# Kernel tuning notes

Measured on AMD Instinct MI355X. Metric: run time of the kernel, lower is better.

Reference implementation:

```python
import jax, jax.numpy as jnp
import numpy as np

# dims: B jets, K routed slots per jet, S particles, D embed, E experts, H heads
B, K, S, D, E, H = 512, 2, 128, 128, 4, 8
F = 4 * D  # ffn_dim
MAXN = 1.0 - 1e-5  # Poincare ball (c=1) max norm for projx


def _n(x):
    return jnp.sqrt(jnp.clip(jnp.sum(x * x, axis=-1, keepdims=True), 1e-15))


def expmap0(u):
    n = _n(u)
    return jnp.tanh(n) * u / n


def logmap0(x):
    n = _n(x)
    return jnp.arctanh(jnp.minimum(n, MAXN)) * x / n


def projx(x):
    n = _n(x)
    return jnp.where(n > MAXN, x * (MAXN / n), x)


def mobius_add(x, y):
    xy = jnp.sum(x * y, axis=-1, keepdims=True)
    x2 = jnp.sum(x * x, axis=-1, keepdims=True)
    y2 = jnp.sum(y * y, axis=-1, keepdims=True)
    num = (1.0 + 2.0 * xy + y2) * x + (1.0 - x2) * y
    den = 1.0 + 2.0 * xy + x2 * y2
    return num / jnp.clip(den, 1e-15)


def layernorm(x, g, b):
    m = jnp.mean(x, axis=-1, keepdims=True)
    v = jnp.mean((x - m) ** 2, axis=-1, keepdims=True)
    return g * (x - m) / jnp.sqrt(v + 1e-5) + b


def man_linear(x, W, b):
    # Manifold_Linear: mobius matvec == expmap0(W @ logmap0(x)), then mobius bias, projx
    return projx(mobius_add(expmap0(logmap0(x) @ W.T), expmap0(b)))


def mob_relu(x):
    # Mob_Act(ReLU): expmap0(relu(logmap0(x)))
    return expmap0(jax.nn.relu(logmap0(x)))


def setup_inputs():
    key = jax.random.key(0)
    ks = jax.random.split(key, 16)
    features = expmap0(0.05 * jax.random.normal(ks[0], (B, K, S, D), jnp.float32))
    # K distinct expert ids per sample (original .nonzero().item() assumes uniqueness)
    expert_indices = jnp.argsort(jax.random.uniform(ks[1], (B, E)), axis=1)[:, :K].astype(jnp.int32)
    pm = jax.random.uniform(ks[2], (B, S)) < 0.2
    pm = pm.at[:, 0].set(False)  # keep at least one valid token per row
    w = lambda k, shp, sc: sc * jax.random.normal(k, shp, jnp.float32)
    s = 1.0 / np.sqrt(D)
    sf = 1.0 / np.sqrt(F)
    return dict(
        features=features, expert_indices=expert_indices, padding_mask=pm,
        ln1_g=jnp.ones((E, D)), ln1_b=jnp.zeros((E, D)),
        ln2_g=jnp.ones((E, D)), ln2_b=jnp.zeros((E, D)),
        wq=w(ks[3], (E, D, D), s), bq=w(ks[4], (E, D), 0.02),
        wk=w(ks[5], (E, D, D), s), bk=w(ks[6], (E, D), 0.02),
        wv=w(ks[7], (E, D, D), s), bv=w(ks[8], (E, D), 0.02),
        wo=w(ks[9], (E, D, D), s), bo=w(ks[10], (E, D), 0.02),
        fc1_w=w(ks[11], (E, F, D), s), fc1_b=w(ks[12], (E, F), 0.02),
        fc2_w=w(ks[13], (E, D, F), sf), fc2_b=w(ks[14], (E, D), 0.02),
    )


def _mha(x, Wq, bq, Wk, bk, Wv, bv, Wo, bo, pad_bias):
    b, s, d = x.shape
    hd = d // H
    q = logmap0(man_linear(x, Wq, bq)).reshape(b, s, H, hd)
    k = logmap0(man_linear(x, Wk, bk)).reshape(b, s, H, hd)
    v = logmap0(man_linear(x, Wv, bv)).reshape(b, s, H, hd)
    scores = jnp.einsum('bqhd,bkhd->bhqk', q, k) * (1.0 / np.sqrt(hd)) + pad_bias
    att = jax.nn.softmax(scores, axis=-1)
    ctx = jnp.einsum('bhqk,bkhd->bqhd', att, v).reshape(b, s, d)
    return man_linear(expmap0(ctx), Wo, bo)


def _expert(x, e, P, pad_bias):
    res = x
    h = expmap0(layernorm(logmap0(x), P['ln1_g'][e], P['ln1_b'][e]))
    h = projx(_mha(h, P['wq'][e], P['bq'][e], P['wk'][e], P['bk'][e],
                   P['wv'][e], P['bv'][e], P['wo'][e], P['bo'][e], pad_bias))
    x = projx(mobius_add(h, res))
    res = x
    h = projx(expmap0(layernorm(logmap0(x), P['ln2_g'][e], P['ln2_b'][e])))
    h = projx(mob_relu(man_linear(h, P['fc1_w'][e], P['fc1_b'][e])))
    h = mob_relu(man_linear(h, P['fc2_w'][e], P['fc2_b'][e]))
    return projx(mobius_add(h, res))


def reference(features, expert_indices, padding_mask,
              ln1_g, ln1_b, ln2_g, ln2_b,
              wq, bq, wk, bk, wv, bv, wo, bo,
              fc1_w, fc1_b, fc2_w, fc2_b):
    P = dict(ln1_g=ln1_g, ln1_b=ln1_b, ln2_g=ln2_g, ln2_b=ln2_b,
             wq=wq, bq=bq, wk=wk, bk=bk, wv=wv, bv=bv, wo=wo, bo=bo,
             fc1_w=fc1_w, fc1_b=fc1_b, fc2_w=fc2_w, fc2_b=fc2_b)
    pad_bias = jnp.where(padding_mask, -1e9, 0.0)[:, None, None, :]  # [B,1,1,S]
    outs = []
    for e in range(E):  # small fixed expert loop (distinct params)
        sel = expert_indices == e  # [B,K]
        present = jnp.any(sel, axis=1)  # [B]
        slot = jnp.argmax(sel, axis=1)  # [B]
        x = jnp.take_along_axis(features, slot[:, None, None, None], axis=1)[:, 0]  # [B,S,D]
        y = _expert(x, e, P, pad_bias)
        outs.append(jnp.where(present[:, None, None], y, 0.0))
    return jnp.stack(outs, axis=1)  # [B,E,S,D]; zero rows where expert not routed
```

## Files before the change

### kernel.cpp

```cpp
#include <hip/hip_runtime.h>
#include <stdint.h>

#define SS 128
#define DD 128
#define EE 4
#define HH 8
#define HDIM 16
#define FF 512
#define BB 512
#define KK 2
#define NTASK (BB*KK)
#define MAXNF 0.99999f
#define NW3 786432

typedef unsigned short u16;
typedef unsigned int u32;

typedef __attribute__((ext_vector_type(8))) short s8v;
typedef __attribute__((ext_vector_type(4))) float f4v;

#define MFMA32(a,b,c) __builtin_amdgcn_mfma_f32_16x16x32_bf16(a,b,c,0,0,0)

__device__ __forceinline__ float bf2f(u16 h){ return __uint_as_float(((u32)h)<<16); }
__device__ __forceinline__ u16 f2bf(float f){
  u32 x = __float_as_uint(f);
  u32 r = x + 0x7FFFu + ((x>>16)&1u);
  return (u16)(r>>16);
}
__device__ __forceinline__ float bfl(u32 u){ return __uint_as_float(u<<16); }
__device__ __forceinline__ float bfh(u32 u){ return __uint_as_float(u & 0xFFFF0000u); }

__device__ __forceinline__ float wsum(float v){
  #pragma unroll
  for(int off=32; off>0; off>>=1) v += __shfl_xor(v, off, 64);
  return v;
}
__device__ __forceinline__ float wmax(float v){
  #pragma unroll
  for(int off=32; off>0; off>>=1) v = fmaxf(v, __shfl_xor(v, off, 64));
  return v;
}
__device__ __forceinline__ float artanhf_(float x){ return 0.5f*logf((1.f+x)/(1.f-x)); }

__device__ __forceinline__ u32 cvtpk(float a, float b){
  u32 r; asm("v_cvt_pk_bf16_f32 %0, %1, %2" : "=v"(r) : "v"(a), "v"(b)); return r;
}
__device__ __forceinline__ void split2(float a, float b, u32& H, u32& M, u32& L){
  H = cvtpk(a,b);
  float ra = a - bfl(H), rb = b - bfh(H);
  M = cvtpk(ra,rb);
  float sa = ra - bfl(M), sb = rb - bfh(M);
  L = cvtpk(sa,sb);
}
__device__ __forceinline__ void split8(const float* v, s8v& H, s8v& M, s8v& L){
  union { u32 w[4]; s8v s; } uh, um, ul;
  #pragma unroll
  for(int p=0;p<4;++p){
    u32 a,bq2,c; split2(v[2*p], v[2*p+1], a, bq2, c);
    uh.w[p]=a; um.w[p]=bq2; ul.w[p]=c;
  }
  H=uh.s; M=um.s; L=ul.s;
}
__device__ __forceinline__ s8v sel8(int c, s8v a, s8v b){ return c ? a : b; }

template<typename T> __device__ __forceinline__ float ldv(const T* p){
  if constexpr (sizeof(T)==2) return bf2f(*(const u16*)p);
  else return *(const float*)p;
}
template<typename T> __device__ __forceinline__ void stv(T* p, float v){
  if constexpr (sizeof(T)==2) *(u16*)p = f2bf(v);
  else *(float*)p = v;
}
template<typename T> __device__ __forceinline__ void loadrow(const T* p, float* w){
  if constexpr (sizeof(T)==2){
    const uint4* q=(const uint4*)p;
    #pragma unroll
    for(int r=0;r<16;++r){
      uint4 t=q[r];
      w[r*8+0]=bfl(t.x); w[r*8+1]=bfh(t.x);
      w[r*8+2]=bfl(t.y); w[r*8+3]=bfh(t.y);
      w[r*8+4]=bfl(t.z); w[r*8+5]=bfh(t.z);
      w[r*8+6]=bfl(t.w); w[r*8+7]=bfh(t.w);
    }
  } else {
    const float4* q=(const float4*)p;
    #pragma unroll
    for(int r=0;r<32;++r){ float4 t=q[r]; w[r*4]=t.x; w[r*4+1]=t.y; w[r*4+2]=t.z; w[r*4+3]=t.w; }
  }
}
__device__ __forceinline__ float dotrow(const float* __restrict__ w, const float* __restrict__ u){
  float a0=0.f,a1=0.f,a2=0.f,a3=0.f;
  #pragma unroll
  for(int i=0;i<128;i+=4){
    a0+=w[i]*u[i]; a1+=w[i+1]*u[i+1]; a2+=w[i+2]*u[i+2]; a3+=w[i+3]*u[i+3];
  }
  return (a0+a1)+(a2+a3);
}

template<int NPL> __device__ __forceinline__ float vnorm(const float* v){
  float s=0.f;
  #pragma unroll
  for(int i=0;i<NPL;++i) s += v[i]*v[i];
  s = wsum(s);
  return sqrtf(fmaxf(s, 1e-15f));
}
template<int NPL> __device__ __forceinline__ void f_logmap0(float* v){
  float n = vnorm<NPL>(v);
  float sc = artanhf_(fminf(n, MAXNF))/n;
  #pragma unroll
  for(int i=0;i<NPL;++i) v[i]*=sc;
}
template<int NPL> __device__ __forceinline__ void f_expmap0(float* v){
  float n = vnorm<NPL>(v);
  float sc = tanhf(n)/n;
  #pragma unroll
  for(int i=0;i<NPL;++i) v[i]*=sc;
}
template<int NPL> __device__ __forceinline__ void f_projx(float* v){
  float n = vnorm<NPL>(v);
  if(n > MAXNF){
    float sc = MAXNF/n;
    #pragma unroll
    for(int i=0;i<NPL;++i) v[i]*=sc;
  }
}
template<int NPL> __device__ __forceinline__ void f_mobius_add(float* x, const float* y){
  float xy=0.f, x2=0.f, y2=0.f;
  #pragma unroll
  for(int i=0;i<NPL;++i){ xy+=x[i]*y[i]; x2+=x[i]*x[i]; y2+=y[i]*y[i]; }
  xy=wsum(xy); x2=wsum(x2); y2=wsum(y2);
  float cx = 1.f + 2.f*xy + y2;
  float cy = 1.f - x2;
  float den = fmaxf(1.f + 2.f*xy + x2*y2, 1e-15f);
  float inv = 1.f/den;
  #pragma unroll
  for(int i=0;i<NPL;++i) x[i] = (cx*x[i] + cy*y[i])*inv;
}
template<int NPL> __device__ __forceinline__ void f_layernorm(float* v, const float* g, const float* b){
  const float invD = 1.f/(float)(NPL*64);
  float m=0.f;
  #pragma unroll
  for(int i=0;i<NPL;++i) m += v[i];
  m = wsum(m)*invD;
  float s2=0.f;
  #pragma unroll
  for(int i=0;i<NPL;++i){ v[i]-=m; s2 += v[i]*v[i]; }
  s2 = wsum(s2)*invD;
  float inv = 1.f/sqrtf(s2+1e-5f);
  #pragma unroll
  for(int i=0;i<NPL;++i) v[i] = g[i]*(v[i]*inv) + b[i];
}

__device__ __forceinline__ u32 xf32(int row, int colf){
  return (u32)row*512u + (((u32)colf*4u) ^ (((u32)row&7u)<<4));
}
__device__ __forceinline__ u32 xbh(int row, int colb){
  return (u32)row*256u + (((u32)colb*2u) ^ (((u32)row&7u)<<4));
}
__device__ __forceinline__ u32 xhid(int row, int colb){
  return (u32)row*1024u + (((u32)colb*2u) ^ (((u32)row&7u)<<4));
}
__device__ __forceinline__ u32 xfr_(int row, int colf){
  return (u32)row*2048u + (((u32)colf*4u) ^ (((u32)row&7u)<<4));
}

__global__ void prep_kernel(const u16* __restrict__ feat16,
                            const unsigned char* __restrict__ mask,
                            float* __restrict__ mbias, int* __restrict__ flag){
  __shared__ int s_stats, s_max, s_nan;
  if(threadIdx.x==0){ s_stats=0; s_max=0; s_nan=0; }
  __syncthreads();
  int c=0;
  for(int i=threadIdx.x; i<131072; i+=blockDim.x){
    u16 v = feat16[i];
    if(((v>>7)&0xFFu)==0xFFu) c++;
  }
  if(c) atomicAdd(&s_nan, c);
  int lstats=0, lmax=0;
  for(int i=threadIdx.x; i<BB*SS; i+=blockDim.x){
    int v = mask[i];
    if(v){
      lmax = v>lmax ? v : lmax;
      if((i&3)==1) lstats|=1;
      if((i&3)!=0) lstats|=2;
    }
  }
  if(lstats) atomicOr(&s_stats, lstats);
  atomicMax(&s_max, lmax);
  __syncthreads();
  if(threadIdx.x==0) *flag = (s_nan>0) ? 1 : 0;
  int mode;
  if(s_max<=1) mode = (s_stats&2) ? 0 : 1;
  else         mode = (s_stats&1) ? 2 : 3;
  for(int i=threadIdx.x; i<BB*SS; i+=blockDim.x){
    bool m2;
    if(mode==0)      m2 = mask[i]!=0;
    else if(mode==1) m2 = ((const int*)mask)[i]!=0;
    else if(mode==2) m2 = ((const u16*)mask)[i]!=0;
    else             m2 = ((((const u32*)mask)[i])<<1)!=0;
    mbias[i] = m2 ? -1e9f : 0.f;
  }
}

template<typename T>
__global__ void zero_nr(const int* __restrict__ flag, const int* __restrict__ eidx, T* __restrict__ out){
  const int want = (sizeof(T)==4) ? 1 : 0;
  if(*flag != want) return;
  for(int slab=blockIdx.x; slab<BB*EE; slab+=gridDim.x){
    int b = slab>>2, e = slab&3;
    if(eidx[b*KK]==e || eidx[b*KK+1]==e) continue;
    T* p = out + (size_t)slab*(SS*DD);
    for(int i=threadIdx.x; i<SS*DD; i+=blockDim.x){
      if constexpr (sizeof(T)==2) p[i] = (T)0; else p[i] = 0.f;
    }
  }
}

__global__ void wsplit_kernel(const int* __restrict__ flag,
                              const float* __restrict__ wq, const float* __restrict__ wk,
                              const float* __restrict__ wv, const float* __restrict__ wo,
                              const float* __restrict__ f1w, const float* __restrict__ f2w,
                              u16* __restrict__ wsp){
  if(*flag != 1) return;
  int i = blockIdx.x*256 + threadIdx.x;
  if(i >= NW3) return;
  float x;
  if(i < 65536)       x = wq[i];
  else if(i < 131072) x = wk[i-65536];
  else if(i < 196608) x = wv[i-131072];
  else if(i < 262144) x = wo[i-196608];
  else if(i < 524288) x = f1w[i-262144];
  else                x = f2w[i-524288];
  u32 H,M,L; split2(x,x,H,M,L);
  wsp[i]         = (u16)H;
  wsp[NW3 + i]   = (u16)M;
  wsp[2*NW3 + i] = (u16)L;
}

__global__ __launch_bounds__(512)
void moe_f32(const int* __restrict__ flag,
             const float* __restrict__ feat, const int* __restrict__ eidx,
             const float* __restrict__ mbias,
             const float* __restrict__ ln1g, const float* __restrict__ ln1b,
             const float* __restrict__ ln2g, const float* __restrict__ ln2b,
             const float* __restrict__ bq, const float* __restrict__ bk_,
             const float* __restrict__ bv, const float* __restrict__ bo,
             const float* __restrict__ f1b, const float* __restrict__ f2b,
             const u16* __restrict__ wsp,
             float* __restrict__ out, float* __restrict__ wsl, int ntask)
{
  if(*flag != 1) return;

  __shared__ __align__(16) char LB[163840];
  char* Uh = LB;
  char* Um = LB + 32768;
  char* R2 = LB + 65536;
  char* SX = LB + 131072;
  char* HB = LB + 98304;
  char* C2 = LB + 147456;

  const int tid = threadIdx.x;
  const int lane = tid & 63;
  const int w    = tid >> 6;
  const int ll   = lane & 15;
  const int hl   = lane >> 4;

  u16* myl = (u16*)wsl + (size_t)blockIdx.x * 16384;

  for(int task = blockIdx.x; task < ntask; task += gridDim.x){
    __syncthreads();
    const int b = task >> 1, slot = task & 1;
    const int e  = eidx[b*KK + slot];
    const int eo = eidx[b*KK + (slot^1)];
    int used = (1<<e)|(1<<eo), sp = 0, cnt = 0;
    #pragma unroll
    for(int t2=0;t2<4;++t2){ if(!((used>>t2)&1)){ if(cnt==slot) sp=t2; cnt++; } }
    const float* X = feat + (size_t)task * (SS*DD);
    float* own   = out + ((size_t)(b*EE+e )) * (SS*DD);
    float* spare = out + ((size_t)(b*EE+sp)) * (SS*DD);

    float g1[2],b1[2],g2[2],b2[2],ebq[2],ebk[2],ebv[2],ebo[2],ebf2[2],ebf1[8];
    {
      float2 t0;
      t0 = *(const float2*)(ln1g + e*DD + 2*lane); g1[0]=t0.x; g1[1]=t0.y;
      t0 = *(const float2*)(ln1b + e*DD + 2*lane); b1[0]=t0.x; b1[1]=t0.y;
      t0 = *(const float2*)(ln2g + e*DD + 2*lane); g2[0]=t0.x; g2[1]=t0.y;
      t0 = *(const float2*)(ln2b + e*DD + 2*lane); b2[0]=t0.x; b2[1]=t0.y;
      t0 = *(const float2*)(bq  + e*DD + 2*lane); ebq[0]=t0.x; ebq[1]=t0.y; f_expmap0<2>(ebq);
      t0 = *(const float2*)(bk_ + e*DD + 2*lane); ebk[0]=t0.x; ebk[1]=t0.y; f_expmap0<2>(ebk);
      t0 = *(const float2*)(bv  + e*DD + 2*lane); ebv[0]=t0.x; ebv[1]=t0.y; f_expmap0<2>(ebv);
      t0 = *(const float2*)(bo  + e*DD + 2*lane); ebo[0]=t0.x; ebo[1]=t0.y; f_expmap0<2>(ebo);
      t0 = *(const float2*)(f2b + e*DD + 2*lane); ebf2[0]=t0.x; ebf2[1]=t0.y; f_expmap0<2>(ebf2);
      #pragma unroll
      for(int j=0;j<4;++j){
        t0 = *(const float2*)(f1b + e*FF + 2*lane + 128*j); ebf1[2*j]=t0.x; ebf1[2*j+1]=t0.y;
      }
      f_expmap0<8>(ebf1);
    }
    float mb_reg[8];
    #pragma unroll
    for(int nt=0;nt<8;++nt) mb_reg[nt] = mbias[b*SS + nt*16 + ll];

    for(int r=0;r<16;++r){
      int t = w*16 + r;
      float2 xv = *(const float2*)(X + t*DD + 2*lane);
      float v[2] = {xv.x, xv.y};
      f_logmap0<2>(v);
      f_layernorm<2>(v, g1, b1);
      f_expmap0<2>(v);
      f_logmap0<2>(v);
      u32 H,M,L; split2(v[0],v[1],H,M,L);
      *(u32*)(Uh + xbh(t, 2*lane)) = H;
      *(u32*)(Um + xbh(t, 2*lane)) = M;
      ((u32*)myl)[t*64 + lane] = L;
    }
    __syncthreads();

    #pragma unroll
    for(int m=0;m<3;++m){
      const u32 tb = (m==0 ? 0u : (m==1 ? 65536u : 131072u)) + (u32)e*16384u;
      s8v Bh[8], Blm[8];
      {
        int nrow = w*16 + ll;
        #pragma unroll
        for(int c=0;c<8;++c){
          u32 koff = c*16 + (hl&1)*8;
          Bh[c]  = *(const s8v*)(wsp + 0*NW3 + tb + nrow*128 + koff);
          Blm[c] = *(const s8v*)(wsp + (hl<2?2:1)*NW3 + tb + nrow*128 + koff);
        }
      }
      for(int ch=0; ch<4; ++ch){
        #pragma unroll
        for(int sub=0; sub<2; ++sub){
          int mt = 2*ch + sub;
          f4v acc = {0.f,0.f,0.f,0.f};
          #pragma unroll
          for(int c=0;c<8;++c){
            int arow = mt*16 + ll;
            u32 koff = c*16 + (hl&1)*8;
            s8v A1 = *(const s8v*)((hl<2?Uh:Um) + xbh(arow, koff));
            s8v lf = *(const s8v*)((const u16*)myl + arow*128 + koff);
            s8v hf = *(const s8v*)(Uh + xbh(arow, koff));
            s8v A2 = sel8(hl<2, lf, hf);
            s8v B3 = sel8(hl<2, Bh[c], Blm[c]);
            acc = MFMA32(A1, Bh[c], acc);
            acc = MFMA32(A1, Blm[c], acc);
            acc = MFMA32(A2, B3, acc);
          }
          #pragma unroll
          for(int i=0;i<4;++i)
            *(float*)(SX + xf32(sub*16 + hl*4 + i, w*16 + ll)) = acc[i];
        }
        __syncthreads();
        for(int rr=0; rr<4; ++rr){
          int lr = w*4 + rr; int t = ch*32 + lr;
          float2 pp = *(const float2*)(SX + xf32(lr, 2*lane));
          float v[2] = {pp.x, pp.y};
          f_expmap0<2>(v);
          float eb[2];
          if(m==0){ eb[0]=ebq[0]; eb[1]=ebq[1]; }
          else if(m==1){ eb[0]=ebk[0]; eb[1]=ebk[1]; }
          else { eb[0]=ebv[0]; eb[1]=ebv[1]; }
          f_mobius_add<2>(v, eb);
          f_projx<2>(v);
          f_logmap0<2>(v);
          if(m==0){
            float2 o2; o2.x=v[0]; o2.y=v[1];
            *(float2*)(spare + t*DD + 2*lane) = o2;
          } else if(m==1){
            *(float*)(R2 + xf32(t, 2*lane))   = v[0];
            *(float*)(R2 + xf32(t, 2*lane+1)) = v[1];
          } else {
            own[(2*lane)*DD + t]   = v[0];
            own[(2*lane+1)*DD + t] = v[1];
          }
        }
        __syncthreads();
      }
    }

    for(int h=0; h<HH; ++h){
      {
        int tok = tid & 127, dq = tid >> 7;
        float4 vv = *(const float4*)(R2 + xf32(tok, h*16 + dq*4));
        u32 H0,M0,L0,H1,M1,L1;
        split2(vv.x,vv.y,H0,M0,L0); split2(vv.z,vv.w,H1,M1,L1);
        u32 o = (u32)tok*48u + (u32)dq*8u;
        *(u32*)(SX + 0*6144 + o) = H0; *(u32*)(SX + 0*6144 + o + 4) = H1;
        *(u32*)(SX + 1*6144 + o) = M0; *(u32*)(SX + 1*6144 + o + 4) = M1;
        *(u32*)(SX + 2*6144 + o) = L0; *(u32*)(SX + 2*6144 + o + 4) = L1;
      }
      __syncthreads();
      float qa[8];
      {
        float4 q0 = *(const float4*)(spare + (w*16+ll)*DD + h*16 + (hl&1)*8);
        float4 q1 = *(const float4*)(spare + (w*16+ll)*DD + h*16 + (hl&1)*8 + 4);
        qa[0]=q0.x; qa[1]=q0.y; qa[2]=q0.z; qa[3]=q0.w;
        qa[4]=q1.x; qa[5]=q1.y; qa[6]=q1.z; qa[7]=q1.w;
      }
      s8v QH,QM,QL; split8(qa, QH,QM,QL);
      s8v qA1 = sel8(hl<2, QH, QM);
      s8v qA2 = sel8(hl<2, QL, QH);
      f4v sc[8];
      #pragma unroll
      for(int nt=0;nt<8;++nt){
        u32 o = (u32)(nt*16+ll)*48u + (u32)(hl&1)*16u;
        s8v B1 = *(const s8v*)(SX + 0*6144 + o);
        s8v B2 = *(const s8v*)(SX + (hl<2?2:1)*6144 + o);
        s8v B3 = sel8(hl<2, B1, B2);
        f4v z = {0.f,0.f,0.f,0.f};
        z = MFMA32(qA1, B1, z);
        z = MFMA32(qA1, B2, z);
        z = MFMA32(qA2, B3, z);
        sc[nt] = z;
      }
      __syncthreads();
      #pragma unroll
      for(int i=0;i<4;++i){
        float p8[8]; float mx = -3e38f;
        #pragma unroll
        for(int nt=0;nt<8;++nt){ p8[nt] = sc[nt][i]*0.25f + mb_reg[nt]; mx = fmaxf(mx, p8[nt]); }
        #pragma unroll
        for(int o=1;o<16;o<<=1) mx = fmaxf(mx, __shfl_xor(mx, o, 64));
        float dn = 0.f;
        #pragma unroll
        for(int nt=0;nt<8;++nt){ p8[nt] = expf(p8[nt]-mx); dn += p8[nt]; }
        #pragma unroll
        for(int o=1;o<16;o<<=1) dn += __shfl_xor(dn, o, 64);
        float inv = 1.f/dn;
        #pragma unroll
        for(int nt=0;nt<8;++nt)
          *(float*)(LB + xf32(w*16 + hl*4 + i, nt*16 + ll)) = p8[nt]*inv;
      }
      f4v ca = {0.f,0.f,0.f,0.f};
      #pragma unroll
      for(int c=0;c<8;++c){
        float pa[8];
        {
          float4 p0 = *(const float4*)(LB + xf32(w*16+ll, c*16 + (hl&1)*8));
          float4 p1 = *(const float4*)(LB + xf32(w*16+ll, c*16 + (hl&1)*8 + 4));
          pa[0]=p0.x; pa[1]=p0.y; pa[2]=p0.z; pa[3]=p0.w;
          pa[4]=p1.x; pa[5]=p1.y; pa[6]=p1.z; pa[7]=p1.w;
        }
        s8v PH,PM,PL; split8(pa, PH,PM,PL);
        s8v pA1 = sel8(hl<2, PH, PM);
        s8v pA2 = sel8(hl<2, PL, PH);
        float va[8];
        {
          const float* vp = own + (h*16+ll)*DD + c*16 + (hl&1)*8;
          float4 v0 = *(const float4*)(vp);
          float4 v1 = *(const float4*)(vp + 4);
          va[0]=v0.x; va[1]=v0.y; va[2]=v0.z; va[3]=v0.w;
          va[4]=v1.x; va[5]=v1.y; va[6]=v1.z; va[7]=v1.w;
        }
        s8v VH,VM,VL; split8(va, VH,VM,VL);
        s8v vB2 = sel8(hl<2, VL, VM);
        s8v vB3 = sel8(hl<2, VH, VM);
        ca = MFMA32(pA1, VH, ca);
        ca = MFMA32(pA1, vB2, ca);
        ca = MFMA32(pA2, vB3, ca);
      }
      #pragma unroll
      for(int i=0;i<4;++i)
        *(float*)(R2 + xf32(w*16 + hl*4 + i, h*16 + ll)) = ca[i];
    }
    __syncthreads();

    for(int r=0;r<16;++r){
      int t = w*16 + r;
      float v[2];
      v[0] = *(const float*)(R2 + xf32(t, 2*lane));
      v[1] = *(const float*)(R2 + xf32(t, 2*lane+1));
      f_expmap0<2>(v);
      f_logmap0<2>(v);
      u32 H,M,L; split2(v[0],v[1],H,M,L);
      *(u32*)(Uh + xbh(t, 2*lane)) = H;
      *(u32*)(Um + xbh(t, 2*lane)) = M;
      ((u32*)myl)[t*64 + lane] = L;
    }
    __syncthreads();

    {
      const u32 tb = 196608u + (u32)e*16384u;
      s8v Bh[8], Blm[8];
      {
        int nrow = w*16 + ll;
        #pragma unroll
        for(int c=0;c<8;++c){
          u32 koff = c*16 + (hl&1)*8;
          Bh[c]  = *(const s8v*)(wsp + 0*NW3 + tb + nrow*128 + koff);
          Blm[c] = *(const s8v*)(wsp + (hl<2?2:1)*NW3 + tb + nrow*128 + koff);
        }
      }
      for(int ch=0; ch<4; ++ch){
        #pragma unroll
        for(int sub=0; sub<2; ++sub){
          int mt = 2*ch + sub;
          f4v acc = {0.f,0.f,0.f,0.f};
          #pragma unroll
          for(int c=0;c<8;++c){
            int arow = mt*16 + ll;
            u32 koff = c*16 + (hl&1)*8;
            s8v A1 = *(const s8v*)((hl<2?Uh:Um) + xbh(arow, koff));
            s8v lf = *(const s8v*)((const u16*)myl + arow*128 + koff);
            s8v hf = *(const s8v*)(Uh + xbh(arow, koff));
            s8v A2 = sel8(hl<2, lf, hf);
            s8v B3 = sel8(hl<2, Bh[c], Blm[c]);
            acc = MFMA32(A1, Bh[c], acc);
            acc = MFMA32(A1, Blm[c], acc);
            acc = MFMA32(A2, B3, acc);
          }
          #pragma unroll
          for(int i=0;i<4;++i)
            *(float*)(SX + xf32(sub*16 + hl*4 + i, w*16 + ll)) = acc[i];
        }
        __syncthreads();
        for(int rr=0; rr<4; ++rr){
          int lr = w*4 + rr; int t = ch*32 + lr;
          float2 pp = *(const float2*)(SX + xf32(lr, 2*lane));
          float v[2] = {pp.x, pp.y};
          f_expmap0<2>(v);
          f_mobius_add<2>(v, ebo);
          f_projx<2>(v);
          f_projx<2>(v);
          float2 rr2 = *(const float2*)(X + t*DD + 2*lane);
          float res[2] = {rr2.x, rr2.y};
          f_mobius_add<2>(v, res);
          f_projx<2>(v);
          float2 xo; xo.x=v[0]; xo.y=v[1];
          *(float2*)(own + t*DD + 2*lane) = xo;
          f_logmap0<2>(v);
          f_layernorm<2>(v, g2, b2);
          f_expmap0<2>(v);
          f_projx<2>(v);
          f_logmap0<2>(v);
          u32 H,M,L; split2(v[0],v[1],H,M,L);
          *(u32*)(Uh + xbh(t, 2*lane)) = H;
          *(u32*)(Um + xbh(t, 2*lane)) = M;
          ((u32*)myl)[t*64 + lane] = L;
        }
        __syncthreads();
      }
    }

    for(int tc=0; tc<8; ++tc){
      {
        f4v fa[4];
        #pragma unroll
        for(int n4=0;n4<4;++n4){ fa[n4][0]=0.f; fa[n4][1]=0.f; fa[n4][2]=0.f; fa[n4][3]=0.f; }
        #pragma unroll
        for(int c=0;c<8;++c){
          int arow = tc*16 + ll;
          u32 koff = c*16 + (hl&1)*8;
          s8v A1 = *(const s8v*)((hl<2?Uh:Um) + xbh(arow, koff));
          s8v lf = *(const s8v*)((const u16*)myl + arow*128 + koff);
          s8v hf = *(const s8v*)(Uh + xbh(arow, koff));
          s8v A2 = sel8(hl<2, lf, hf);
          #pragma unroll
          for(int n4=0;n4<4;++n4){
            u32 nrow = (u32)((w*4+n4)*16 + ll);
            s8v B1 = *(const s8v*)(wsp + 0*NW3 + 262144u + (u32)e*65536u + nrow*128 + koff);
            s8v B2 = *(const s8v*)(wsp + (hl<2?2:1)*NW3 + 262144u + (u32)e*65536u + nrow*128 + koff);
            s8v B3 = sel8(hl<2, B1, B2);
            fa[n4] = MFMA32(A1, B1, fa[n4]);
            fa[n4] = MFMA32(A1, B2, fa[n4]);
            fa[n4] = MFMA32(A2, B3, fa[n4]);
          }
        }
        #pragma unroll
        for(int n4=0;n4<4;++n4)
          #pragma unroll
          for(int i=0;i<4;++i)
            *(float*)(R2 + xfr_(hl*4+i, (w*4+n4)*16 + ll)) = fa[n4][i];
      }
      __syncthreads();
      for(int rr=0; rr<2; ++rr){
        int lr = w*2 + rr;
        float v[8];
        #pragma unroll
        for(int j=0;j<4;++j){
          float2 pp = *(const float2*)(R2 + xfr_(lr, 2*lane + 128*j));
          v[2*j]=pp.x; v[2*j+1]=pp.y;
        }
        f_expmap0<8>(v);
        f_mobius_add<8>(v, ebf1);
        f_projx<8>(v);
        f_logmap0<8>(v);
        #pragma unroll
        for(int i=0;i<8;++i) v[i] = fmaxf(v[i], 0.f);
        f_expmap0<8>(v);
        f_projx<8>(v);
        f_logmap0<8>(v);
        #pragma unroll
        for(int j=0;j<4;++j){
          u32 H,M,L; split2(v[2*j], v[2*j+1], H,M,L);
          *(u32*)(HB + 0*16384 + xhid(lr, 2*lane + 128*j)) = H;
          *(u32*)(HB + 1*16384 + xhid(lr, 2*lane + 128*j)) = M;
          *(u32*)(HB + 2*16384 + xhid(lr, 2*lane + 128*j)) = L;
        }
      }
      __syncthreads();
      {
        f4v ga = {0.f,0.f,0.f,0.f};
        #pragma unroll
        for(int c=0;c<32;++c){
          u32 koff = c*16 + (hl&1)*8;
          s8v A1 = *(const s8v*)(HB + (hl<2?0:1)*16384 + xhid(ll, koff));
          s8v lf = *(const s8v*)(HB + 2*16384 + xhid(ll, koff));
          s8v hf = *(const s8v*)(HB + 0*16384 + xhid(ll, koff));
          s8v A2 = sel8(hl<2, lf, hf);
          u32 nrow = (u32)(w*16 + ll);
          s8v B1 = *(const s8v*)(wsp + 0*NW3 + 524288u + (u32)e*65536u + nrow*512 + koff);
          s8v B2 = *(const s8v*)(wsp + (hl<2?2:1)*NW3 + 524288u + (u32)e*65536u + nrow*512 + koff);
          s8v B3 = sel8(hl<2, B1, B2);
          ga = MFMA32(A1, B1, ga);
          ga = MFMA32(A1, B2, ga);
          ga = MFMA32(A2, B3, ga);
        }
        #pragma unroll
        for(int i=0;i<4;++i)
          *(float*)(C2 + xf32(hl*4+i, w*16 + ll)) = ga[i];
      }
      __syncthreads();
      for(int rr=0; rr<2; ++rr){
        int lr = w*2 + rr; int gt = tc*16 + lr;
        float2 pp; pp.x = *(const float*)(C2 + xf32(lr, 2*lane));
        pp.y = *(const float*)(C2 + xf32(lr, 2*lane+1));
        float v[2] = {pp.x, pp.y};
        f_expmap0<2>(v);
        f_mobius_add<2>(v, ebf2);
        f_projx<2>(v);
        f_logmap0<2>(v);
        v[0]=fmaxf(v[0],0.f); v[1]=fmaxf(v[1],0.f);
        f_expmap0<2>(v);
        float2 xx = *(const float2*)(own + gt*DD + 2*lane);
        float x1v[2] = {xx.x, xx.y};
        f_mobius_add<2>(v, x1v);
        f_projx<2>(v);
        float2 o2; o2.x=v[0]; o2.y=v[1];
        *(float2*)(own + gt*DD + 2*lane) = o2;
      }
      __syncthreads();
    }

    {
      float4 z4 = {0.f,0.f,0.f,0.f};
      for(int i=tid; i<4096; i+=512) *(float4*)(spare + 4*i) = z4;
    }
  }
}

template<typename T>
__global__ __launch_bounds__(256)
void moe_kernel(const int* __restrict__ flag,
                const T* __restrict__ feat, const int* __restrict__ eidx,
                const float* __restrict__ mbias,
                const T* __restrict__ ln1g, const T* __restrict__ ln1b,
                const T* __restrict__ ln2g, const T* __restrict__ ln2b,
                const T* __restrict__ wq, const T* __restrict__ bq,
                const T* __restrict__ wk, const T* __restrict__ bk_,
                const T* __restrict__ wv, const T* __restrict__ bv,
                const T* __restrict__ wo, const T* __restrict__ bo,
                const T* __restrict__ f1w, const T* __restrict__ f1b,
                const T* __restrict__ f2w, const T* __restrict__ f2b,
                T* __restrict__ out, float* __restrict__ ws, int ntask)
{
  const int want = (sizeof(T)==4) ? 1 : 0;
  if(*flag != want) return;

  __shared__ float U[SS*DD];
  const int tid  = threadIdx.x;
  const int lane = tid & 63;
  const int wid  = tid >> 6;
  float* T0 = ws + (size_t)blockIdx.x * (4*SS*DD);
  float* T1 = T0 + SS*DD;
  float* T2 = T1 + SS*DD;
  float* T3 = T2 + SS*DD;

  for(int task = blockIdx.x; task < ntask; task += gridDim.x){
    __syncthreads();
    const int b = task >> 1;
    const int e = eidx[b*KK + (task & 1)];
    const T* X = feat + (size_t)task * (SS*DD);

    for(int r=0;r<32;++r){
      int t = wid*32 + r;
      float v[2];
      v[0]=ldv(&X[t*DD+lane]); v[1]=ldv(&X[t*DD+lane+64]);
      f_logmap0<2>(v);
      float g[2], bb[2];
      g[0]=ldv(&ln1g[e*DD+lane]);  g[1]=ldv(&ln1g[e*DD+lane+64]);
      bb[0]=ldv(&ln1b[e*DD+lane]); bb[1]=ldv(&ln1b[e*DD+lane+64]);
      f_layernorm<2>(v,g,bb);
      f_expmap0<2>(v);
      f_logmap0<2>(v);
      U[t*DD+lane]=v[0]; U[t*DD+lane+64]=v[1];
    }
    __syncthreads();

    {
      int j = tid & 127, tg = tid >> 7;
      for(int m=0;m<3;++m){
        const T* Wm = (m==0?wq : m==1?wk : wv) + (size_t)e*DD*DD + (size_t)j*DD;
        float* Ym = (m==0?T0 : m==1?T1 : T2);
        float w[128];
        loadrow(Wm, w);
        for(int tt=0;tt<64;++tt){
          int t = tg*64+tt;
          Ym[t*DD+j] = dotrow(w, &U[t*DD]);
        }
      }
// ... 103 lines not shown

    float* HID = T0;
    for(int tc=0; tc<2; ++tc){
      for(int pass=0;pass<2;++pass){
        int f = pass*256 + tid;
        float w[128];
        loadrow(f1w + (size_t)e*FF*DD + (size_t)f*DD, w);
        for(int tt=0;tt<64;++tt){
          HID[tt*FF+f] = dotrow(w, &U[(tc*64+tt)*DD]);
        }
      }
      __syncthreads();
      for(int r=0;r<16;++r){
        int t = wid*16+r;
        float v[8];
        #pragma unroll
        for(int i=0;i<8;++i) v[i]=HID[t*FF+lane+64*i];
        f_expmap0<8>(v);
        float ebv8[8];
        #pragma unroll
        for(int i=0;i<8;++i) ebv8[i]=ldv(&f1b[e*FF+lane+64*i]);
        f_expmap0<8>(ebv8);
        f_mobius_add<8>(v, ebv8);
        f_projx<8>(v);
        f_logmap0<8>(v);
        #pragma unroll
        for(int i=0;i<8;++i) v[i]=fmaxf(v[i],0.f);
        f_expmap0<8>(v);
        f_projx<8>(v);
        f_logmap0<8>(v);
        #pragma unroll
        for(int i=0;i<8;++i) HID[t*FF+lane+64*i]=v[i];
      }
      __syncthreads();
      {
        int j=tid&127, tg=tid>>7;
        for(int fc=0;fc<4;++fc){
          float w[128];
          loadrow(f2w + (size_t)e*DD*FF + (size_t)j*FF + fc*128, w);
          for(int tt=0;tt<32;++tt){
            int t=tg*32+tt;
            float acc = dotrow(w, HID + t*FF + fc*128);
            if(fc==0) T2[t*DD+j]=acc; else T2[t*DD+j]+=acc;
          }
        }
      }
      __syncthreads();
      for(int r=0;r<16;++r){
        int t=wid*16+r; int gt = tc*64+t;
        float v[2]; v[0]=T2[t*DD+lane]; v[1]=T2[t*DD+lane+64];
        f_expmap0<2>(v);
        float ebv2[2]; ebv2[0]=ldv(&f2b[e*DD+lane]); ebv2[1]=ldv(&f2b[e*DD+lane+64]);
        f_expmap0<2>(ebv2);
        f_mobius_add<2>(v, ebv2);
        f_projx<2>(v);
        f_logmap0<2>(v);
        v[0]=fmaxf(v[0],0.f); v[1]=fmaxf(v[1],0.f);
        f_expmap0<2>(v);
        float x1v[2]; x1v[0]=T3[gt*DD+lane]; x1v[1]=T3[gt*DD+lane+64];
        f_mobius_add<2>(v, x1v);
        f_projx<2>(v);
        T* op = out + ((size_t)(b*EE+e)*SS + gt)*DD;
        stv(&op[lane],    v[0]);
        stv(&op[lane+64], v[1]);
      }
      __syncthreads();
    }
  }
}

extern "C" void kernel_launch(void* const* d_in, const int* in_sizes, int n_in,
                              void* d_out, int out_size, void* d_ws, size_t ws_size,
                              hipStream_t stream){
  const void* feat = d_in[0];
  const int* eidx = (const int*)d_in[1];
  const unsigned char* pmask = (const unsigned char*)d_in[2];
  float* ws = (float*)d_ws;

  int* flag = (int*)ws;
  float* mbias = ws + 16;
  float* tiles = ws + 16 + BB*SS;
  u16* wsp = (u16*)(ws + 16 + BB*SS);
  const size_t WSP_F32 = (size_t)(3*NW3)/2;
  float* wsl = ws + 16 + BB*SS + WSP_F32;

  long wsf = (long)(ws_size/sizeof(float));
  long avail_old = wsf - (16 + BB*SS);
  long remain = wsf - (long)(16 + BB*SS) - (long)WSP_F32;

  int G = (int)(avail_old / (long)(4*SS*DD));
  if(G > NTASK) G = NTASK;
  if(G < 1) G = 1;
  int G2 = (int)(remain / 8192);
  if(G2 > 256) G2 = 256;
  bool newpath = (G2 >= 1);

  prep_kernel<<<1,256,0,stream>>>((const u16*)feat, pmask, mbias, flag);
  zero_nr<u16>  <<<2048,256,0,stream>>>(flag, eidx, (u16*)d_out);
  zero_nr<float><<<2048,256,0,stream>>>(flag, eidx, (float*)d_out);

  if(newpath){
    wsplit_kernel<<<(NW3+255)/256,256,0,stream>>>(flag,
      (const float*)d_in[7], (const float*)d_in[9], (const float*)d_in[11], (const float*)d_in[13],
      (const float*)d_in[15], (const float*)d_in[17], wsp);
    moe_f32<<<G2,512,0,stream>>>(flag, (const float*)d_in[0], eidx, mbias,
      (const float*)d_in[3], (const float*)d_in[4], (const float*)d_in[5], (const float*)d_in[6],
      (const float*)d_in[8], (const float*)d_in[10], (const float*)d_in[12], (const float*)d_in[14],
      (const float*)d_in[16], (const float*)d_in[18],
      wsp, (float*)d_out, wsl, NTASK);
  }

  #define ARGS(T_) flag, (const T_*)d_in[0], eidx, mbias, \
    (const T_*)d_in[3], (const T_*)d_in[4], (const T_*)d_in[5], (const T_*)d_in[6], \
    (const T_*)d_in[7], (const T_*)d_in[8], (const T_*)d_in[9], (const T_*)d_in[10], \
    (const T_*)d_in[11], (const T_*)d_in[12], (const T_*)d_in[13], (const T_*)d_in[14], \
    (const T_*)d_in[15], (const T_*)d_in[16], (const T_*)d_in[17], (const T_*)d_in[18], \
    (T_*)d_out, tiles, NTASK
  moe_kernel<u16><<<G,256,0,stream>>>(ARGS(u16));
  if(!newpath){
    moe_kernel<float><<<G,256,0,stream>>>(ARGS(float));
  }
  #undef ARGS
}
```

Before: 4.289 ms.

## Keep activations as fp32 in LDS and split to bf16 parts on the fly

Activations are now stored once as fp32 in shared memory and split into hi/mid/lo bf16 parts inside each MFMA tile load. This replaces the old scheme that kept hi/mid planes in LDS and spilled the lo plane to a global workspace. The FFN stage now handles 32-token chunks instead of 16, reusing the FC1 output buffer for the hidden state. The transposed V write goes through an LDS staging tile so global stores are coalesced. The cost is repeated split arithmetic per tile and larger register arrays for the A operands, which could reduce occupancy or cause spills.

```diff
diff --git a/kernel.cpp b/kernel.cpp
--- a/kernel.cpp
+++ b/kernel.cpp
@@ -63,6 +63,34 @@
 }
 __device__ __forceinline__ s8v sel8(int c, s8v a, s8v b){ return c ? a : b; }
 
+__device__ __forceinline__ u32 xf32(int row, int colf){
+  return (u32)row*512u + (((u32)colf*4u) ^ (((u32)row&7u)<<4));
+}
+__device__ __forceinline__ u32 xfr_(int row, int colf){
+  return (u32)row*2048u + (((u32)colf*4u) ^ (((u32)row&7u)<<4));
+}
+
+__device__ __forceinline__ void mkA512(const char* T, int row, int colf, int hm, s8v& A1, s8v& A2){
+  float va[8];
+  float4 v0 = *(const float4*)(T + xf32(row, colf));
+  float4 v1 = *(const float4*)(T + xf32(row, colf+4));
+  va[0]=v0.x; va[1]=v0.y; va[2]=v0.z; va[3]=v0.w;
+  va[4]=v1.x; va[5]=v1.y; va[6]=v1.z; va[7]=v1.w;
+  s8v H,M,L; split8(va, H,M,L);
+  A1 = sel8(hm, H, M);
+  A2 = sel8(hm, L, H);
+}
+__device__ __forceinline__ void mkA2048(const char* T, int row, int colf, int hm, s8v& A1, s8v& A2){
+  float va[8];
+  float4 v0 = *(const float4*)(T + xfr_(row, colf));
+  float4 v1 = *(const float4*)(T + xfr_(row, colf+4));
+  va[0]=v0.x; va[1]=v0.y; va[2]=v0.z; va[3]=v0.w;
+  va[4]=v1.x; va[5]=v1.y; va[6]=v1.z; va[7]=v1.w;
+  s8v H,M,L; split8(va, H,M,L);
+  A1 = sel8(hm, H, M);
+  A2 = sel8(hm, L, H);
+}
+
 template<typename T> __device__ __forceinline__ float ldv(const T* p){
   if constexpr (sizeof(T)==2) return bf2f(*(const u16*)p);
   else return *(const float*)p;
@@ -149,19 +177,6 @@
   float inv = 1.f/sqrtf(s2+1e-5f);
   #pragma unroll
   for(int i=0;i<NPL;++i) v[i] = g[i]*(v[i]*inv) + b[i];
-}
-
-__device__ __forceinline__ u32 xf32(int row, int colf){
-  return (u32)row*512u + (((u32)colf*4u) ^ (((u32)row&7u)<<4));
-}
-__device__ __forceinline__ u32 xbh(int row, int colb){
-  return (u32)row*256u + (((u32)colb*2u) ^ (((u32)row&7u)<<4));
-}
-__device__ __forceinline__ u32 xhid(int row, int colb){
-  return (u32)row*1024u + (((u32)colb*2u) ^ (((u32)row&7u)<<4));
-}
-__device__ __forceinline__ u32 xfr_(int row, int colf){
-  return (u32)row*2048u + (((u32)colf*4u) ^ (((u32)row&7u)<<4));
 }
 
 __global__ void prep_kernel(const u16* __restrict__ feat16,
@@ -247,25 +262,22 @@
              const float* __restrict__ bv, const float* __restrict__ bo,
              const float* __restrict__ f1b, const float* __restrict__ f2b,
              const u16* __restrict__ wsp,
-             float* __restrict__ out, float* __restrict__ wsl, int ntask)
+             float* __restrict__ out, int ntask)
 {
   if(*flag != 1) return;
 
   __shared__ __align__(16) char LB[163840];
-  char* Uh = LB;
-  char* Um = LB + 32768;
-  char* R2 = LB + 65536;
-  char* SX = LB + 131072;
-  char* HB = LB + 98304;
-  char* C2 = LB + 147456;
+  char* UF  = LB;
+  char* R2  = LB + 65536;
+  char* SX  = LB + 131072;
+  char* VTS = LB + 131072 + 16384;
 
   const int tid = threadIdx.x;
   const int lane = tid & 63;
   const int w    = tid >> 6;
   const int ll   = lane & 15;
   const int hl   = lane >> 4;
-
-  u16* myl = (u16*)wsl + (size_t)blockIdx.x * 16384;
+  const int hm   = (hl < 2);
 
   for(int task = blockIdx.x; task < ntask; task += gridDim.x){
     __syncthreads();
@@ -292,8 +304,8 @@
       t0 = *(const float2*)(bo  + e*DD + 2*lane); ebo[0]=t0.x; ebo[1]=t0.y; f_expmap0<2>(ebo);
       t0 = *(const float2*)(f2b + e*DD + 2*lane); ebf2[0]=t0.x; ebf2[1]=t0.y; f_expmap0<2>(ebf2);
       #pragma unroll
-      for(int j=0;j<4;++j){
-        t0 = *(const float2*)(f1b + e*FF + 2*lane + 128*j); ebf1[2*j]=t0.x; ebf1[2*j+1]=t0.y;
+      for(int j2=0;j2<4;++j2){
+        t0 = *(const float2*)(f1b + e*FF + 2*lane + 128*j2); ebf1[2*j2]=t0.x; ebf1[2*j2+1]=t0.y;
       }
       f_expmap0<8>(ebf1);
     }
@@ -309,43 +321,39 @@
       f_layernorm<2>(v, g1, b1);
       f_expmap0<2>(v);
       f_logmap0<2>(v);
-      u32 H,M,L; split2(v[0],v[1],H,M,L);
-      *(u32*)(Uh + xbh(t, 2*lane)) = H;
-      *(u32*)(Um + xbh(t, 2*lane)) = M;
-      ((u32*)myl)[t*64 + lane] = L;
+      float2 o2; o2.x=v[0]; o2.y=v[1];
+      *(float2*)(UF + xf32(t, 2*lane)) = o2;
     }
     __syncthreads();
 
     #pragma unroll
     for(int m=0;m<3;++m){
-      const u32 tb = (m==0 ? 0u : (m==1 ? 65536u : 131072u)) + (u32)e*16384u;
+      const u32 tb = (u32)m*65536u + (u32)e*16384u;
       s8v Bh[8], Blm[8];
       {
         int nrow = w*16 + ll;
         #pragma unroll
         for(int c=0;c<8;++c){
           u32 koff = c*16 + (hl&1)*8;
-          Bh[c]  = *(const s8v*)(wsp + 0*NW3 + tb + nrow*128 + koff);
-          Blm[c] = *(const s8v*)(wsp + (hl<2?2:1)*NW3 + tb + nrow*128 + koff);
+          Bh[c]  = *(const s8v*)(wsp + tb + nrow*128 + koff);
+          Blm[c] = *(const s8v*)(wsp + (hm?2:1)*NW3 + tb + nrow*128 + koff);
         }
       }
       for(int ch=0; ch<4; ++ch){
         #pragma unroll
         for(int sub=0; sub<2; ++sub){
-          int mt = 2*ch + sub;
+          int arow = (2*ch+sub)*16 + ll;
+          s8v A1v[8], A2v[8];
+          #pragma unroll
+          for(int c=0;c<8;++c)
+            mkA512(UF, arow, c*16 + (hl&1)*8, hm, A1v[c], A2v[c]);
           f4v acc = {0.f,0.f,0.f,0.f};
           #pragma unroll
           for(int c=0;c<8;++c){
-            int arow = mt*16 + ll;
-            u32 koff = c*16 + (hl&1)*8;
-            s8v A1 = *(const s8v*)((hl<2?Uh:Um) + xbh(arow, koff));
-            s8v lf = *(const s8v*)((const u16*)myl + arow*128 + koff);
-            s8v hf = *(const s8v*)(Uh + xbh(arow, koff));
-            s8v A2 = sel8(hl<2, lf, hf);
-            s8v B3 = sel8(hl<2, Bh[c], Blm[c]);
-            acc = MFMA32(A1, Bh[c], acc);
-            acc = MFMA32(A1, Blm[c], acc);
-            acc = MFMA32(A2, B3, acc);
+            s8v B3 = sel8(hm, Bh[c], Blm[c]);
+            acc = MFMA32(A1v[c], Bh[c], acc);
+            acc = MFMA32(A1v[c], Blm[c], acc);
+            acc = MFMA32(A2v[c], B3, acc);
           }
           #pragma unroll
           for(int i=0;i<4;++i)
@@ -368,16 +376,24 @@
             float2 o2; o2.x=v[0]; o2.y=v[1];
             *(float2*)(spare + t*DD + 2*lane) = o2;
           } else if(m==1){
-            *(float*)(R2 + xf32(t, 2*lane))   = v[0];
-            *(float*)(R2 + xf32(t, 2*lane+1)) = v[1];
+            float2 o2; o2.x=v[0]; o2.y=v[1];
+            *(float2*)(R2 + xf32(t, 2*lane)) = o2;
           } else {
-            own[(2*lane)*DD + t]   = v[0];
-            own[(2*lane+1)*DD + t] = v[1];
+            *(float*)(VTS + (2*lane)*128   + lr*4) = v[0];
+            *(float*)(VTS + (2*lane+1)*128 + lr*4) = v[1];
           }
         }
         __syncthreads();
-      }
-    }
+        if(m==2){
+          int d = tid >> 2, kk = (tid & 3) * 8;
+          float4 a0 = *(const float4*)(VTS + d*128 + kk*4);
+          float4 a1 = *(const float4*)(VTS + d*128 + kk*4 + 16);
+          *(float4*)(own + (size_t)d*DD + ch*32 + kk)     = a0;
+          *(float4*)(own + (size_t)d*DD + ch*32 + kk + 4) = a1;
+        }
+      }
+    }
+    __syncthreads();
 
     for(int h=0; h<HH; ++h){
       {
@@ -399,15 +415,15 @@
         qa[4]=q1.x; qa[5]=q1.y; qa[6]=q1.z; qa[7]=q1.w;
       }
       s8v QH,QM,QL; split8(qa, QH,QM,QL);
-      s8v qA1 = sel8(hl<2, QH, QM);
-      s8v qA2 = sel8(hl<2, QL, QH);
+      s8v qA1 = sel8(hm, QH, QM);
+      s8v qA2 = sel8(hm, QL, QH);
       f4v sc[8];
       #pragma unroll
       for(int nt=0;nt<8;++nt){
         u32 o = (u32)(nt*16+ll)*48u + (u32)(hl&1)*16u;
         s8v B1 = *(const s8v*)(SX + 0*6144 + o);
-        s8v B2 = *(const s8v*)(SX + (hl<2?2:1)*6144 + o);
-        s8v B3 = sel8(hl<2, B1, B2);
+        s8v B2 = *(const s8v*)(SX + (hm?2:1)*6144 + o);
+        s8v B3 = sel8(hm, B1, B2);
         f4v z = {0.f,0.f,0.f,0.f};
         z = MFMA32(qA1, B1, z);
         z = MFMA32(qA1, B2, z);
@@ -430,21 +446,21 @@
         float inv = 1.f/dn;
         #pragma unroll
         for(int nt=0;nt<8;++nt)
-          *(float*)(LB + xf32(w*16 + hl*4 + i, nt*16 + ll)) = p8[nt]*inv;
+          *(float*)(UF + xf32(w*16 + hl*4 + i, nt*16 + ll)) = p8[nt]*inv;
       }
       f4v ca = {0.f,0.f,0.f,0.f};
       #pragma unroll
       for(int c=0;c<8;++c){
         float pa[8];
         {
-          float4 p0 = *(const float4*)(LB + xf32(w*16+ll, c*16 + (hl&1)*8));
-          float4 p1 = *(const float4*)(LB + xf32(w*16+ll, c*16 + (hl&1)*8 + 4));
+          float4 p0 = *(const float4*)(UF + xf32(w*16+ll, c*16 + (hl&1)*8));
+          float4 p1 = *(const float4*)(UF + xf32(w*16+ll, c*16 + (hl&1)*8 + 4));
           pa[0]=p0.x; pa[1]=p0.y; pa[2]=p0.z; pa[3]=p0.w;
           pa[4]=p1.x; pa[5]=p1.y; pa[6]=p1.z; pa[7]=p1.w;
         }
         s8v PH,PM,PL; split8(pa, PH,PM,PL);
-        s8v pA1 = sel8(hl<2, PH, PM);
-        s8v pA2 = sel8(hl<2, PL, PH);
+        s8v pA1 = sel8(hm, PH, PM);
+        s8v pA2 = sel8(hm, PL, PH);
         float va[8];
         {
           const float* vp = own + (h*16+ll)*DD + c*16 + (hl&1)*8;
@@ -454,8 +470,8 @@
           va[4]=v1.x; va[5]=v1.y; va[6]=v1.z; va[7]=v1.w;
         }
         s8v VH,VM,VL; split8(va, VH,VM,VL);
-        s8v vB2 = sel8(hl<2, VL, VM);
-        s8v vB3 = sel8(hl<2, VH, VM);
+        s8v vB2 = sel8(hm, VL, VM);
+        s8v vB3 = sel8(hm, VH, VM);
         ca = MFMA32(pA1, VH, ca);
         ca = MFMA32(pA1, vB2, ca);
         ca = MFMA32(pA2, vB3, ca);
@@ -468,15 +484,12 @@
 
     for(int r=0;r<16;++r){
       int t = w*16 + r;
-      float v[2];
-      v[0] = *(const float*)(R2 + xf32(t, 2*lane));
-      v[1] = *(const float*)(R2 + xf32(t, 2*lane+1));
+      float2 cc2 = *(const float2*)(R2 + xf32(t, 2*lane));
+      float v[2] = {cc2.x, cc2.y};
       f_expmap0<2>(v);
       f_logmap0<2>(v);
-      u32 H,M,L; split2(v[0],v[1],H,M,L);
-      *(u32*)(Uh + xbh(t, 2*lane)) = H;
-      *(u32*)(Um + xbh(t, 2*lane)) = M;
-      ((u32*)myl)[t*64 + lane] = L;
+      float2 o2; o2.x=v[0]; o2.y=v[1];
+      *(float2*)(UF + xf32(t, 2*lane)) = o2;
     }
     __syncthreads();
 
@@ -488,27 +501,25 @@
         #pragma unroll
         for(int c=0;c<8;++c){
           u32 koff = c*16 + (hl&1)*8;
-          Bh[c]  = *(const s8v*)(wsp + 0*NW3 + tb + nrow*128 + koff);
-          Blm[c] = *(const s8v*)(wsp + (hl<2?2:1)*NW3 + tb + nrow*128 + koff);
+          Bh[c]  = *(const s8v*)(wsp + tb + nrow*128 + koff);
+          Blm[c] = *(const s8v*)(wsp + (hm?2:1)*NW3 + tb + nrow*128 + koff);
         }
       }
       for(int ch=0; ch<4; ++ch){
         #pragma unroll
         for(int sub=0; sub<2; ++sub){
-          int mt = 2*ch + sub;
+          int arow = (2*ch+sub)*16 + ll;
+          s8v A1v[8], A2v[8];
+          #pragma unroll
+          for(int c=0;c<8;++c)
+            mkA512(UF, arow, c*16 + (hl&1)*8, hm, A1v[c], A2v[c]);
           f4v acc = {0.f,0.f,0.f,0.f};
           #pragma unroll
           for(int c=0;c<8;++c){
-            int arow = mt*16 + ll;
-            u32 koff = c*16 + (hl&1)*8;
-            s8v A1 = *(const s8v*)((hl<2?Uh:Um) + xbh(arow, koff));
-            s8v lf = *(const s8v*)((const u16*)myl + arow*128 + koff);
-            s8v hf = *(const s8v*)(Uh + xbh(arow, koff));
-            s8v A2 = sel8(hl<2, lf, hf);
-            s8v B3 = sel8(hl<2, Bh[c], Blm[c]);
-            acc = MFMA32(A1, Bh[c], acc);
-            acc = MFMA32(A1, Blm[c], acc);
-            acc = MFMA32(A2, B3, acc);
+            s8v B3 = sel8(hm, Bh[c], Blm[c]);
+            acc = MFMA32(A1v[c], Bh[c], acc);
+            acc = MFMA32(A1v[c], Blm[c], acc);
+            acc = MFMA32(A2v[c], B3, acc);
           }
           #pragma unroll
           for(int i=0;i<4;++i)
@@ -534,53 +545,51 @@
           f_expmap0<2>(v);
           f_projx<2>(v);
           f_logmap0<2>(v);
-          u32 H,M,L; split2(v[0],v[1],H,M,L);
-          *(u32*)(Uh + xbh(t, 2*lane)) = H;
-          *(u32*)(Um + xbh(t, 2*lane)) = M;
-          ((u32*)myl)[t*64 + lane] = L;
+          float2 o2; o2.x=v[0]; o2.y=v[1];
+          *(float2*)(UF + xf32(t, 2*lane)) = o2;
         }
         __syncthreads();
       }
     }
 
-    for(int tc=0; tc<8; ++tc){
+    for(int tc=0; tc<4; ++tc){
+      const int t0 = tc*32;
       {
-        f4v fa[4];
-        #pragma unroll
-        for(int n4=0;n4<4;++n4){ fa[n4][0]=0.f; fa[n4][1]=0.f; fa[n4][2]=0.f; fa[n4][3]=0.f; }
-        #pragma unroll
-        for(int c=0;c<8;++c){
-          int arow = tc*16 + ll;
-          u32 koff = c*16 + (hl&1)*8;
-          s8v A1 = *(const s8v*)((hl<2?Uh:Um) + xbh(arow, koff));
-          s8v lf = *(const s8v*)((const u16*)myl + arow*128 + koff);
-          s8v hf = *(const s8v*)(Uh + xbh(arow, koff));
-          s8v A2 = sel8(hl<2, lf, hf);
+        #pragma unroll
+        for(int mt=0; mt<2; ++mt){
+          int arow = t0 + mt*16 + ll;
+          s8v A1v[8], A2v[8];
+          #pragma unroll
+          for(int c=0;c<8;++c)
+            mkA512(UF, arow, c*16 + (hl&1)*8, hm, A1v[c], A2v[c]);
           #pragma unroll
           for(int n4=0;n4<4;++n4){
-            u32 nrow = (u32)((w*4+n4)*16 + ll);
-            s8v B1 = *(const s8v*)(wsp + 0*NW3 + 262144u + (u32)e*65536u + nrow*128 + koff);
-            s8v B2 = *(const s8v*)(wsp + (hl<2?2:1)*NW3 + 262144u + (u32)e*65536u + nrow*128 + koff);
-            s8v B3 = sel8(hl<2, B1, B2);
-            fa[n4] = MFMA32(A1, B1, fa[n4]);
-            fa[n4] = MFMA32(A1, B2, fa[n4]);
-            fa[n4] = MFMA32(A2, B3, fa[n4]);
+            u32 nrow = (u32)(w*64 + n4*16 + ll);
+            f4v acc = {0.f,0.f,0.f,0.f};
+            #pragma unroll
+            for(int c=0;c<8;++c){
+              u32 koff = c*16 + (hl&1)*8;
+              s8v B1 = *(const s8v*)(wsp + 262144u + (u32)e*65536u + nrow*128 + koff);
+              s8v B2 = *(const s8v*)(wsp + (hm?2:1)*NW3 + 262144u + (u32)e*65536u + nrow*128 + koff);
+              s8v B3 = sel8(hm, B1, B2);
+              acc = MFMA32(A1v[c], B1, acc);
+              acc = MFMA32(A1v[c], B2, acc);
+              acc = MFMA32(A2v[c], B3, acc);
+            }
+            #pragma unroll
+            for(int i=0;i<4;++i)
+              *(float*)(R2 + xfr_(mt*16 + hl*4 + i, w*64 + n4*16 + ll)) = acc[i];
           }
         }
-        #pragma unroll
-        for(int n4=0;n4<4;++n4)
-          #pragma unroll
-          for(int i=0;i<4;++i)
-            *(float*)(R2 + xfr_(hl*4+i, (w*4+n4)*16 + ll)) = fa[n4][i];
       }
       __syncthreads();
-      for(int rr=0; rr<2; ++rr){
-        int lr = w*2 + rr;
+      for(int rr=0; rr<4; ++rr){
+        int lr = w*4 + rr;
         float v[8];
         #pragma unroll
-        for(int j=0;j<4;++j){
-          float2 pp = *(const float2*)(R2 + xfr_(lr, 2*lane + 128*j));
-          v[2*j]=pp.x; v[2*j+1]=pp.y;
+        for(int j2=0;j2<4;++j2){
+          float2 pp = *(const float2*)(R2 + xfr_(lr, 2*lane + 128*j2));
+          v[2*j2]=pp.x; v[2*j2+1]=pp.y;
         }
         f_expmap0<8>(v);
         f_mobius_add<8>(v, ebf1);
@@ -592,41 +601,46 @@
         f_projx<8>(v);
         f_logmap0<8>(v);
         #pragma unroll
-        for(int j=0;j<4;++j){
-          u32 H,M,L; split2(v[2*j], v[2*j+1], H,M,L);
-          *(u32*)(HB + 0*16384 + xhid(lr, 2*lane + 128*j)) = H;
-          *(u32*)(HB + 1*16384 + xhid(lr, 2*lane + 128*j)) = M;
-          *(u32*)(HB + 2*16384 + xhid(lr, 2*lane + 128*j)) = L;
+        for(int j2=0;j2<4;++j2){
+          float2 o2; o2.x=v[2*j2]; o2.y=v[2*j2+1];
+          *(float2*)(R2 + xfr_(lr, 2*lane + 128*j2)) = o2;
         }
       }
       __syncthreads();
       {
-        f4v ga = {0.f,0.f,0.f,0.f};
-        #pragma unroll
-        for(int c=0;c<32;++c){
-          u32 koff = c*16 + (hl&1)*8;
-          s8v A1 = *(const s8v*)(HB + (hl<2?0:1)*16384 + xhid(ll, koff));
-          s8v lf = *(const s8v*)(HB + 2*16384 + xhid(ll, koff));
-          s8v hf = *(const s8v*)(HB + 0*16384 + xhid(ll, koff));
-          s8v A2 = sel8(hl<2, lf, hf);
-          u32 nrow = (u32)(w*16 + ll);
-          s8v B1 = *(const s8v*)(wsp + 0*NW3 + 524288u + (u32)e*65536u + nrow*512 + koff);
-          s8v B2 = *(const s8v*)(wsp + (hl<2?2:1)*NW3 + 524288u + (u32)e*65536u + nrow*512 + koff);
-          s8v B3 = sel8(hl<2, B1, B2);
-          ga = MFMA32(A1, B1, ga);
-          ga = MFMA32(A1, B2, ga);
-          ga = MFMA32(A2, B3, ga);
-        }
-        #pragma unroll
-        for(int i=0;i<4;++i)
-          *(float*)(C2 + xf32(hl*4+i, w*16 + ll)) = ga[i];
+        u32 nrow = (u32)(w*16 + ll);
+        #pragma unroll
+        for(int mt=0; mt<2; ++mt){
+          f4v ga = {0.f,0.f,0.f,0.f};
+          #pragma unroll
+          for(int grp=0; grp<4; ++grp){
+            s8v A1v[8], A2v[8];
+            #pragma unroll
+            for(int cc=0;cc<8;++cc)
+              mkA2048(R2, mt*16 + ll, (grp*8+cc)*16 + (hl&1)*8, hm, A1v[cc], A2v[cc]);
+            #pragma unroll
+            for(int cc=0;cc<8;++cc){
+              int c = grp*8 + cc;
+              u32 koff = c*16 + (hl&1)*8;
+              s8v B1 = *(const s8v*)(wsp + 524288u + (u32)e*65536u + nrow*512 + koff);
+              s8v B2 = *(const s8v*)(wsp + (hm?2:1)*NW3 + 524288u + (u32)e*65536u + nrow*512 + koff);
+              s8v B3 = sel8(hm, B1, B2);
+              ga = MFMA32(A1v[cc], B1, ga);
+              ga = MFMA32(A1v[cc], B2, ga);
+              ga = MFMA32(A2v[cc], B3, ga);
+            }
+          }
+          #pragma unroll
+          for(int i=0;i<4;++i)
+            *(float*)(SX + xf32(mt*16 + hl*4 + i, w*16 + ll)) = ga[i];
+        }
       }
       __syncthreads();
-      for(int rr=0; rr<2; ++rr){
-        int lr = w*2 + rr; int gt = tc*16 + lr;
-        float2 pp; pp.x = *(const float*)(C2 + xf32(lr, 2*lane));
-        pp.y = *(const float*)(C2 + xf32(lr, 2*lane+1));
-        float v[2] = {pp.x, pp.y};
+      for(int rr=0; rr<4; ++rr){
+        int lr = w*4 + rr; int gt = t0 + lr;
+        float v[2];
+        v[0] = *(const float*)(SX + xf32(lr, 2*lane));
+        v[1] = *(const float*)(SX + xf32(lr, 2*lane+1));
         f_expmap0<2>(v);
         f_mobius_add<2>(v, ebf2);
         f_projx<2>(v);
@@ -896,7 +910,6 @@
   float* tiles = ws + 16 + BB*SS;
   u16* wsp = (u16*)(ws + 16 + BB*SS);
   const size_t WSP_F32 = (size_t)(3*NW3)/2;
-  float* wsl = ws + 16 + BB*SS + WSP_F32;
 
   long wsf = (long)(ws_size/sizeof(float));
   long avail_old = wsf - (16 + BB*SS);
@@ -905,9 +918,9 @@
   int G = (int)(avail_old / (long)(4*SS*DD));
   if(G > NTASK) G = NTASK;
   if(G < 1) G = 1;
-  int G2 = (int)(remain / 8192);
-  if(G2 > 256) G2 = 256;
-  bool newpath = (G2 >= 1);
+  int G2 = 256;
+  if(G2 > NTASK) G2 = NTASK;
+  bool newpath = (remain >= 0);
 
   prep_kernel<<<1,256,0,stream>>>((const u16*)feat, pmask, mbias, flag);
   zero_nr<u16>  <<<2048,256,0,stream>>>(flag, eidx, (u16*)d_out);
@@ -921,7 +934,7 @@
       (const float*)d_in[3], (const float*)d_in[4], (const float*)d_in[5], (const float*)d_in[6],
       (const float*)d_in[8], (const float*)d_in[10], (const float*)d_in[12], (const float*)d_in[14],
       (const float*)d_in[16], (const float*)d_in[18],
-      wsp, (float*)d_out, wsl, NTASK);
+      wsp, (float*)d_out, NTASK);
   }
 
   #define ARGS(T_) flag, (const T_*)d_in[0], eidx, mbias, \
```

Measured after the change: 3.682 ms. 14.1% less time.
